# Optimization experiments

Measured on AMD Instinct MI355X. Metric: run time of the kernel, lower is better.

## Reference

```python
import jax, jax.numpy as jnp
import numpy as np

B, S, H = 4, 2048, 1024
E, K, INTER = 16, 2, 512
ALPHA, LIMIT = 1.702, 7.0


def setup_inputs() -> dict:
    key = jax.random.key(0)
    ks = jax.random.split(key, 6)
    return {
        "hidden_states": jax.random.normal(ks[0], (B, S, H), jnp.float32),
        "router_weight": jax.random.normal(ks[1], (H, E), jnp.float32) * 0.02,
        "gate_up_proj": jax.random.normal(ks[2], (E, H, 2 * INTER), jnp.float32) * 0.02,
        "gate_up_proj_bias": jax.random.normal(ks[3], (E, 2 * INTER), jnp.float32) * 0.02,
        "down_proj": jax.random.normal(ks[4], (E, INTER, H), jnp.float32) * 0.02,
        "down_proj_bias": jax.random.normal(ks[5], (E, H), jnp.float32) * 0.02,
    }


def reference(hidden_states, router_weight, gate_up_proj, gate_up_proj_bias,
              down_proj, down_proj_bias):
    b, s, h = hidden_states.shape
    x = hidden_states.reshape(-1, h)  # [T, H]
    # Router: linear logits -> top-k -> softmax over selected -> sparse scores [T, E]
    logits = x @ router_weight                      # [T, E]
    topk_w, topk_i = jax.lax.top_k(logits, K)       # [T, K]
    topk_w = jax.nn.softmax(topk_w, axis=-1)
    one_hot = (topk_i[..., None] == jnp.arange(E)[None, None, :]).astype(topk_w.dtype)
    scores = jnp.einsum('tk,tke->te', topk_w, one_hot)  # [T, E]
    # Fused gate+up projection per expert (num_devices=1 => dispatch/combine identity)
    gu = jnp.einsum('th,ehf->tef', x, gate_up_proj) + gate_up_proj_bias  # [T, E, 2I]
    gate = gu[..., ::2]   # interleaved layout
    up = gu[..., 1::2]
    # gpt_oss activation: clamp + scaled sigmoid glu
    gate = jnp.minimum(gate, LIMIT)
    up = jnp.clip(up, -LIMIT, LIMIT)
    glu = gate * jax.nn.sigmoid(gate * ALPHA)
    act = (up + 1.0) * glu                          # [T, E, I]
    # Down projection + score-weighted combine
    out = jnp.einsum('tei,eih,te->th', act, down_proj, scores)
    out = out + jnp.einsum('te,eh->th', scores, down_proj_bias)
    return out.reshape(b, s, h)
```

## Files before the change

kernel.cpp:

```cpp
#include <hip/hip_runtime.h>
#include <hip/hip_bf16.h>
#include <math.h>

#define TOK   8192
#define HDIM  1024
#define NE    16
#define NI    512
#define F2    1024
#define CAP   8192
#define CAP2  2048
#define ALPHA 1.702f
#define LIMIT 7.0f

typedef __attribute__((ext_vector_type(8))) short short8;
typedef __attribute__((ext_vector_type(4))) short short4v;
typedef __attribute__((ext_vector_type(4))) float f32x4;

static __device__ __forceinline__ unsigned short f2bf(float f) {
    unsigned int u = __float_as_uint(f);
    u += 0x7FFFu + ((u >> 16) & 1u);
    return (unsigned short)(u >> 16);
}
static __device__ __forceinline__ float bf2f(unsigned short u) {
    return __uint_as_float((unsigned int)u << 16);
}

#define GLD_LDS16(g, l) __builtin_amdgcn_global_load_lds(                     \
    (const __attribute__((address_space(1))) void*)(g),                       \
    (__attribute__((address_space(3))) void*)(l), 16, 0, 0)

static __device__ __forceinline__ void do_transpose256(
    const float* __restrict__ in, unsigned short* __restrict__ out,
    int R, int C, int perm, int e, int bx, int by, char* smem, int tid)
{
    unsigned short (*t2)[264] = (unsigned short (*)[264])smem;
    const float* pin = in + (size_t)e * R * C;
    unsigned short* pout = out + (size_t)e * R * C;
    int c0 = bx * 64, r0 = by * 256;

#pragma unroll
    for (int j = 0; j < 8; ++j) {
        int idx = j * 256 + tid;
        int rp = idx >> 4, c4 = (idx & 15) * 4;
        int swz = ((c4 >> 2) & 7) << 3;
        const float* p0 = pin + (size_t)(r0 + 2 * rp) * C + c0 + c4;
        float4 v0 = *(const float4*)(p0);
        float4 v1 = *(const float4*)(p0 + C);
        unsigned int u0 = (unsigned int)f2bf(v0.x) | ((unsigned int)f2bf(v1.x) << 16);
        unsigned int u1 = (unsigned int)f2bf(v0.y) | ((unsigned int)f2bf(v1.y) << 16);
        unsigned int u2 = (unsigned int)f2bf(v0.z) | ((unsigned int)f2bf(v1.z) << 16);
        unsigned int u3 = (unsigned int)f2bf(v0.w) | ((unsigned int)f2bf(v1.w) << 16);
        int kc = (2 * rp) ^ swz;
        *(unsigned int*)&t2[c4 + 0][kc] = u0;
        *(unsigned int*)&t2[c4 + 1][kc] = u1;
        *(unsigned int*)&t2[c4 + 2][kc] = u2;
        *(unsigned int*)&t2[c4 + 3][kc] = u3;
    }
    __syncthreads();

#pragma unroll
    for (int j = 0; j < 8; ++j) {
        int idx = j * 256 + tid;
        int n = idx >> 5, k0 = (idx & 31) * 8;
        int rswz = ((n >> 2) & 7) << 3;
        short8 v = *(const short8*)&t2[n][k0 ^ rswz];
        int c = c0 + n;
        int orow;
        if (perm) {
            int tile = c >> 7, ct = c & 127;
            int fl = ct >> 1, h = ct & 1;
            orow = (tile << 7) | ((fl >> 4) << 5) | (h << 4) | (fl & 15);
        } else {
            orow = c;
        }
        *(short8*)(pout + (size_t)orow * R + r0 + k0) = v;
    }
}

__global__ __launch_bounds__(256) void prep_kernel(
    const float* __restrict__ x, const float* __restrict__ rw,
    const float* __restrict__ gup,
    double* __restrict__ part, unsigned short* __restrict__ xbf,
    unsigned short* __restrict__ gupT)
{
    __shared__ __align__(16) char smem[33792];
    int bid = blockIdx.x;
    int tid = threadIdx.x;

    if (bid >= 512) {
        int i = bid - 512;
        do_transpose256(gup, gupT, HDIM, F2, 1, i >> 6, i & 15, (i >> 4) & 3, smem, tid);
        return;
    }

    int idx = bid;
    int w = tid >> 6;
    int lane = tid & 63;
    int tt = lane & 15, eg = lane >> 4;
    int t0 = idx * 16;
    int hbase = w * 256;

    float* sx  = (float*)(smem + w * 8448);
    float* srw = (float*)(smem + w * 8448 + 4352);

    double acc[4] = {0.0, 0.0, 0.0, 0.0};

    for (int hc = 0; hc < 4; ++hc) {
        int h0 = hbase + hc * 64;
        __syncthreads();
#pragma unroll
        for (int j = 0; j < 4; ++j) {
            int fidx = j * 64 + lane;
            int t = fidx >> 4, c4 = (fidx & 15) * 4;
            float4 v = *(const float4*)(x + (size_t)(t0 + t) * HDIM + h0 + c4);
            *(float4*)&sx[t * 68 + c4] = v;
            short4v s;
            s[0] = (short)f2bf(v.x); s[1] = (short)f2bf(v.y);
            s[2] = (short)f2bf(v.z); s[3] = (short)f2bf(v.w);
            *(short4v*)(xbf + (size_t)(t0 + t) * HDIM + h0 + c4) = s;
        }
#pragma unroll
        for (int j = 0; j < 4; ++j) {
            int ridx = j * 64 + lane;
            int h = ridx >> 2, e4 = (ridx & 3) * 4;
            float4 v = *(const float4*)(rw + (size_t)(h0 + h) * NE + e4);
            *(float4*)&srw[h * 16 + e4] = v;
        }
        __syncthreads();
#pragma unroll 8
        for (int j = 0; j < 64; ++j) {
            float xv = sx[tt * 68 + j];
            float4 wv = *(const float4*)&srw[j * 16 + eg * 4];
            double xd = (double)xv;
            acc[0] += xd * (double)wv.x;
            acc[1] += xd * (double)wv.y;
            acc[2] += xd * (double)wv.z;
            acc[3] += xd * (double)wv.w;
        }
    }
#pragma unroll
    for (int q = 0; q < 4; ++q)
        part[(size_t)(w * NE + eg * 4 + q) * TOK + t0 + tt] = acc[q];
}

__global__ __launch_bounds__(256) void router_combine_kernel(
    const double* __restrict__ part,
    int* __restrict__ counts, int* __restrict__ toks, float* __restrict__ wgts,
    unsigned short* __restrict__ inv)
{
    __shared__ int lhist[NE];
    __shared__ int lbase[NE];
    int tid = threadIdx.x;
    int t = blockIdx.x * 256 + tid;
    if (tid < NE) lhist[tid] = 0;
    __syncthreads();

    double acc[NE];
#pragma unroll
    for (int e = 0; e < NE; ++e)
        acc[e] = part[(size_t)(0 * NE + e) * TOK + t]
               + part[(size_t)(1 * NE + e) * TOK + t]
               + part[(size_t)(2 * NE + e) * TOK + t]
               + part[(size_t)(3 * NE + e) * TOK + t];

    int i0 = 0; double v0 = acc[0];
#pragma unroll
    for (int e = 1; e < NE; ++e) if (acc[e] > v0) { v0 = acc[e]; i0 = e; }
    int i1 = -1; double v1 = -1e300;
#pragma unroll
    for (int e = 0; e < NE; ++e) if (e != i0 && acc[e] > v1) { v1 = acc[e]; i1 = e; }
    double e1 = exp(v1 - v0);
    float w0 = (float)(1.0 / (1.0 + e1));
    float w1 = (float)(e1 / (1.0 + e1));

    int r0 = atomicAdd(&lhist[i0], 1);
    int r1 = atomicAdd(&lhist[i1], 1);
    __syncthreads();
    if (tid < NE) lbase[tid] = atomicAdd(&counts[tid], lhist[tid]);
    __syncthreads();
    int p0 = lbase[i0] + r0; if (p0 > 2047) p0 = 2047;
    int p1 = lbase[i1] + r1; if (p1 > 2047) p1 = 2047;
    toks[i0 * CAP + p0] = t; wgts[i0 * CAP + p0] = w0;
    toks[i1 * CAP + p1] = t; wgts[i1 * CAP + p1] = w1;
    inv[2 * t]     = (unsigned short)((i0 << 11) | p0);
    inv[2 * t + 1] = (unsigned short)((i1 << 11) | p1);
}

#define KLOOP_BODY(NT, KOFF)                                                          \
    int c0 = 0;                                                                       \
    for (int kb = 0; kb < (NT); ++kb) {                                               \
        if (kb + 2 < (NT)) {                                                          \
            int cpre = c0 + 2; if (cpre >= 3) cpre -= 3;                              \
            _Pragma("unroll")                                                         \
            for (int i = 0; i < 2; ++i) {                                             \
                GLD_LDS16(gaA[i] + (kb + 2) * (KOFF), &As[cpre][w * 32 + i * 16][0]); \
                GLD_LDS16(gaB[i] + (kb + 2) * (KOFF), &Bs[cpre][w * 32 + i * 16][0]); \
            }                                                                         \
            asm volatile("s_waitcnt vmcnt(8)" ::: "memory");                          \
        } else if (kb + 1 < (NT)) {                                                   \
            asm volatile("s_waitcnt vmcnt(4)" ::: "memory");                          \
        } else {                                                                      \
            asm volatile("s_waitcnt vmcnt(0)" ::: "memory");                          \
        }                                                                             \
        __builtin_amdgcn_sched_barrier(0);                                            \
        __builtin_amdgcn_s_barrier();                                                 \
        __builtin_amdgcn_sched_barrier(0);                                            \
        short8 af[4], bfr[4];                                                         \
        _Pragma("unroll")                                                             \
        for (int m = 0; m < 4; ++m) af[m] = *(const short8*)&As[c0][wr * 64 + m * 16 + lr][slt]; \
        _Pragma("unroll")                                                             \
        for (int n = 0; n < 4; ++n) bfr[n] = *(const short8*)&Bs[c0][wc * 64 + n * 16 + lr][slt]; \
        _Pragma("unroll")                                                             \
        for (int m = 0; m < 4; ++m)                                                   \
            _Pragma("unroll")                                                         \
            for (int n = 0; n < 4; ++n)                                               \
                acc[m][n] = __builtin_amdgcn_mfma_f32_16x16x32_bf16(af[m], bfr[n], acc[m][n], 0, 0, 0); \
        asm volatile("s_waitcnt lgkmcnt(0)" ::: "memory");                            \
        __builtin_amdgcn_sched_barrier(0);                                            \
        __builtin_amdgcn_s_barrier();                                                 \
        __builtin_amdgcn_sched_barrier(0);                                            \
        c0 = (c0 + 1 == 3) ? 0 : c0 + 1;                                              \
    }

#define KLOOP_PROLOGUE(KOFF)                                                          \
    _Pragma("unroll")                                                                 \
    for (int i = 0; i < 2; ++i) {                                                     \
        GLD_LDS16(gaA[i], &As[0][w * 32 + i * 16][0]);                                \
        GLD_LDS16(gaB[i], &Bs[0][w * 32 + i * 16][0]);                                \
    }                                                                                 \
    _Pragma("unroll")                                                                 \
    for (int i = 0; i < 2; ++i) {                                                     \
        GLD_LDS16(gaA[i] + (KOFF), &As[1][w * 32 + i * 16][0]);                       \
        GLD_LDS16(gaB[i] + (KOFF), &Bs[1][w * 32 + i * 16][0]);                       \
    }

__global__ __launch_bounds__(256) void gemm1_kernel(
    const unsigned short* __restrict__ xb, const unsigned short* __restrict__ gupT,
    const float* __restrict__ gub,
    const int* __restrict__ counts, const int* __restrict__ toks,
    unsigned short* __restrict__ act, const unsigned short* __restrict__ zp,
    const float* __restrict__ dwn, unsigned short* __restrict__ dwnT)
{
    __shared__ __align__(16) char smem[49664];
    int b = blockIdx.x;
    int tid = threadIdx.x;

    if (b >= 2048) {
        int i = b - 2048;
        do_transpose256(dwn, dwnT, NI, HDIM, 0, i >> 5, i & 15, (i >> 4) & 1, smem, tid);
        return;
    }

    unsigned short (*As)[128][32] = (unsigned short (*)[128][32])smem;
    unsigned short (*Bs)[128][32] = (unsigned short (*)[128][32])(smem + 24576);
    int* rtok = (int*)(smem + 49152);

    int e = b & 15;
    int j = b >> 4;
    int nt = j & 7;
    int mt = j >> 3;
    int cnt = counts[e];
    int row0 = mt * 128;
    if (row0 >= cnt) return;
    int n0 = nt * 128;

    int lane = tid & 63;
    int w = tid >> 6;
    int wr = w >> 1, wc = w & 1;
    int lr = lane & 15, lg = lane >> 4;

    if (tid < 128) {
        int p = row0 + tid;
        rtok[tid] = (p < cnt) ? toks[e * CAP + p] : -1;
    }
    __syncthreads();

    int srow = lane >> 2;
    int scol = (((lane & 3) ^ ((lane >> 3) & 3)) * 8);
    int slt = (lg ^ ((lr >> 1) & 3)) * 8;

    const unsigned short* gaA[2];
    const unsigned short* gaB[2];
    const unsigned short* gupE = gupT + (size_t)e * HDIM * F2;
#pragma unroll
    for (int i = 0; i < 2; ++i) {
        int arow = w * 32 + i * 16 + srow;
        int tk = rtok[arow];
        gaA[i] = (tk >= 0) ? (xb + (size_t)tk * HDIM + scol) : (zp + scol);
        int brow = n0 + w * 32 + i * 16 + srow;
        gaB[i] = gupE + (size_t)brow * HDIM + scol;
    }

    f32x4 acc[4][4];
#pragma unroll
    for (int m = 0; m < 4; ++m)
#pragma unroll
        for (int n = 0; n < 4; ++n) acc[m][n] = (f32x4){0.f, 0.f, 0.f, 0.f};

    KLOOP_PROLOGUE(32)
    KLOOP_BODY(HDIM / 32, 32)

    unsigned short* actE = act + (size_t)e * CAP2 * NI;
    int fbase = nt * 64 + wc * 32;
#pragma unroll
    for (int q = 0; q < 2; ++q) {
        int f = fbase + q * 16 + lr;
        float bg = gub[e * F2 + 2 * f];
        float bu = gub[e * F2 + 2 * f + 1];
#pragma unroll
        for (int m = 0; m < 4; ++m) {
#pragma unroll
            for (int r = 0; r < 4; ++r) {
                float gate = acc[m][2 * q][r] + bg;
                float up   = acc[m][2 * q + 1][r] + bu;
                gate = fminf(gate, LIMIT);
                up   = fminf(fmaxf(up, -LIMIT), LIMIT);
                float glu = gate / (1.0f + __expf(-ALPHA * gate));
                float av  = (up + 1.0f) * glu;
                int row = row0 + wr * 64 + m * 16 + lg * 4 + r;
                actE[(size_t)row * NI + f] = f2bf(av);
            }
        }
    }
}

__global__ __launch_bounds__(256) void gemm2_y_kernel(
    const unsigned short* __restrict__ act, const unsigned short* __restrict__ dwnT,
    const float* __restrict__ dwb,
    const int* __restrict__ counts, const float* __restrict__ wgts,
    unsigned short* __restrict__ y)
{
    int b = blockIdx.x;
    int e = b & 15;
    int j = b >> 4;
    int nt = j & 7;
    int mt = j >> 3;
    int cnt = counts[e];
    int row0 = mt * 128;
    if (row0 >= cnt) return;
    int n0 = nt * 128;

    int base_e = 0;
#pragma unroll
    for (int q = 0; q < NE; ++q) base_e += (q < e) ? counts[q] : 0;

    __shared__ __align__(16) unsigned short As[3][128][32];
    __shared__ __align__(16) unsigned short Bs[3][128][32];
    __shared__ float rwgt[128];

    int tid = threadIdx.x;
    int lane = tid & 63;
    int w = tid >> 6;
    int wr = w >> 1, wc = w & 1;
    int lr = lane & 15, lg = lane >> 4;

    if (tid < 128) {
        int p = row0 + tid;
        rwgt[tid] = (p < cnt) ? wgts[e * CAP + p] : 0.0f;
    }
    __syncthreads();

    int srow = lane >> 2;
    int scol = (((lane & 3) ^ ((lane >> 3) & 3)) * 8);
    int slt = (lg ^ ((lr >> 1) & 3)) * 8;

    const unsigned short* gaA[2];
    const unsigned short* gaB[2];
    const unsigned short* actE = act + (size_t)e * CAP2 * NI;
    const unsigned short* dwnE = dwnT + (size_t)e * HDIM * NI;
#pragma unroll
    for (int i = 0; i < 2; ++i) {
        int arow = row0 + w * 32 + i * 16 + srow;
        gaA[i] = actE + (size_t)arow * NI + scol;
        int brow = n0 + w * 32 + i * 16 + srow;
        gaB[i] = dwnE + (size_t)brow * NI + scol;
    }

    f32x4 acc[4][4];
#pragma unroll
    for (int m = 0; m < 4; ++m)
#pragma unroll
        for (int n = 0; n < 4; ++n) acc[m][n] = (f32x4){0.f, 0.f, 0.f, 0.f};

    KLOOP_PROLOGUE(32)
    KLOOP_BODY(NI / 32, 32)

    unsigned short* yB = y + (size_t)(base_e + row0) * HDIM;
#pragma unroll
    for (int n = 0; n < 4; ++n) {
        int hc = n0 + wc * 64 + n * 16 + lr;
        float db = dwb[e * HDIM + hc];
#pragma unroll
        for (int m = 0; m < 4; ++m) {
#pragma unroll
            for (int r = 0; r < 4; ++r) {
                int rl = wr * 64 + m * 16 + lg * 4 + r;
                if (row0 + rl < cnt)
                    yB[(size_t)rl * HDIM + hc] = f2bf(rwgt[rl] * (acc[m][n][r] + db));
            }
        }
    }
}

__global__ __launch_bounds__(256) void out_combine_kernel(
    const unsigned short* __restrict__ y, const unsigned short* __restrict__ inv,
    const int* __restrict__ counts, float* __restrict__ out)
{
    __shared__ int sbase[NE];
    int tid = threadIdx.x;
    int t = blockIdx.x;
    if (tid == 0) {
        int s = 0;
#pragma unroll
        for (int e = 0; e < NE; ++e) { sbase[e] = s; s += counts[e]; }
    }
    __syncthreads();
    unsigned short v0 = inv[2 * t], v1 = inv[2 * t + 1];
    int s0 = sbase[v0 >> 11] + (v0 & 2047);
    int s1 = sbase[v1 >> 11] + (v1 & 2047);
    short4v a = *(const short4v*)(y + (size_t)s0 * HDIM + tid * 4);
    short4v c = *(const short4v*)(y + (size_t)s1 * HDIM + tid * 4);
    float4 o;
    o.x = bf2f((unsigned short)a[0]) + bf2f((unsigned short)c[0]);
    o.y = bf2f((unsigned short)a[1]) + bf2f((unsigned short)c[1]);
    o.z = bf2f((unsigned short)a[2]) + bf2f((unsigned short)c[2]);
    o.w = bf2f((unsigned short)a[3]) + bf2f((unsigned short)c[3]);
    *(float4*)(out + (size_t)t * HDIM + tid * 4) = o;
}

__global__ __launch_bounds__(256) void router_kernel(
    const float* __restrict__ x, const float* __restrict__ rw,
    int* __restrict__ counts, int* __restrict__ toks, float* __restrict__ wgts)
{
    int gwave = (int)((blockIdx.x * 256 + threadIdx.x) >> 6);
    int lane = threadIdx.x & 63;
    if (gwave >= TOK) return;
    const float* xr = x + (size_t)gwave * HDIM;
    double acc[NE];
#pragma unroll
    for (int e = 0; e < NE; ++e) acc[e] = 0.0;
    for (int i = 0; i < HDIM / 64; ++i) {
        int h = i * 64 + lane;
        double xv = (double)xr[h];
        const float* r = rw + (size_t)h * NE;
#pragma unroll
        for (int e = 0; e < NE; ++e) acc[e] += xv * (double)r[e];
    }
#pragma unroll
    for (int e = 0; e < NE; ++e) {
        double v = acc[e];
#pragma unroll
        for (int off = 32; off > 0; off >>= 1) v += __shfl_xor(v, off);
        acc[e] = v;
    }
    if (lane == 0) {
        int i0 = 0; double v0 = acc[0];
#pragma unroll
        for (int e = 1; e < NE; ++e) if (acc[e] > v0) { v0 = acc[e]; i0 = e; }
        int i1 = -1; double v1 = -1e300;
#pragma unroll
        for (int e = 0; e < NE; ++e) if (e != i0 && acc[e] > v1) { v1 = acc[e]; i1 = e; }
        double e1 = exp(v1 - v0);
        float w0 = (float)(1.0 / (1.0 + e1));
        float w1 = (float)(e1 / (1.0 + e1));
        int p0 = atomicAdd(&counts[i0], 1);
        toks[i0 * CAP + p0] = gwave; wgts[i0 * CAP + p0] = w0;
        int p1 = atomicAdd(&counts[i1], 1);
        toks[i1 * CAP + p1] = gwave; wgts[i1 * CAP + p1] = w1;
    }
}

__global__ __launch_bounds__(256) void moe_kernel(
    const float* __restrict__ x,
    const float* __restrict__ gup, const float* __restrict__ gub,
    const float* __restrict__ dwn, const float* __restrict__ dwb,
    const int* __restrict__ counts, const int* __restrict__ toks,
    const float* __restrict__ wgts, float* __restrict__ out)
{
    int e = blockIdx.y;
    int cnt = counts[e];
    int row0 = blockIdx.x * 64;
    if (row0 >= cnt) return;

    __shared__ __align__(16) unsigned short sA[64][40];
    __shared__ __align__(16) unsigned short sB[64][40];
    __shared__ __align__(16) unsigned short sAct[64][520];
    __shared__ int   rtok[64];
    __shared__ float rwgt[64];

    int tid = threadIdx.x;
    if (tid < 64) {
        int idx = row0 + tid;
        bool v = idx < cnt;
        rtok[tid] = v ? toks[e * CAP + idx] : -1;
        rwgt[tid] = v ? wgts[e * CAP + idx] : 0.0f;
    }
    __syncthreads();

    int lane = tid & 63;
    int w = tid >> 6;
    int wr = w >> 1, wc = w & 1;
    int lr = lane & 15, lg = lane >> 4;
    int ar = tid >> 2, ac0 = (tid & 3) * 8;
    int bk = tid >> 3, bf0 = (tid & 7) * 8;
    const float* gupE = gup + (size_t)e * HDIM * F2;

    for (int nb = 0; nb < F2 / 64; ++nb) {
        f32x4 acc[2][2];
#pragma unroll
        for (int mi = 0; mi < 2; ++mi)
#pragma unroll
            for (int ni = 0; ni < 2; ++ni) acc[mi][ni] = (f32x4){0.f, 0.f, 0.f, 0.f};
        for (int kb = 0; kb < HDIM / 32; ++kb) {
            __syncthreads();
            {
                int tk = rtok[ar];
                short8 vv = {0,0,0,0,0,0,0,0};
                if (tk >= 0) {
                    const float* p = x + (size_t)tk * HDIM + kb * 32 + ac0;
                    float4 u0 = *(const float4*)(p); float4 u1 = *(const float4*)(p + 4);
                    vv[0]=(short)f2bf(u0.x); vv[1]=(short)f2bf(u0.y); vv[2]=(short)f2bf(u0.z); vv[3]=(short)f2bf(u0.w);
                    vv[4]=(short)f2bf(u1.x); vv[5]=(short)f2bf(u1.y); vv[6]=(short)f2bf(u1.z); vv[7]=(short)f2bf(u1.w);
                }
                *(short8*)&sA[ar][ac0] = vv;
            }
            {
                const float* p = gupE + (size_t)(kb * 32 + bk) * F2 + nb * 64 + bf0;
                float4 u0 = *(const float4*)(p); float4 u1 = *(const float4*)(p + 4);
                sB[bf0+0][bk]=f2bf(u0.x); sB[bf0+1][bk]=f2bf(u0.y); sB[bf0+2][bk]=f2bf(u0.z); sB[bf0+3][bk]=f2bf(u0.w);
                sB[bf0+4][bk]=f2bf(u1.x); sB[bf0+5][bk]=f2bf(u1.y); sB[bf0+6][bk]=f2bf(u1.z); sB[bf0+7][bk]=f2bf(u1.w);
            }
            __syncthreads();
            short8 a0 = *(const short8*)&sA[wr*32+lr][lg*8];
            short8 a1 = *(const short8*)&sA[wr*32+16+lr][lg*8];
            short8 b0 = *(const short8*)&sB[wc*32+lr][lg*8];
            short8 b1 = *(const short8*)&sB[wc*32+16+lr][lg*8];
            acc[0][0] = __builtin_amdgcn_mfma_f32_16x16x32_bf16(a0,b0,acc[0][0],0,0,0);
            acc[0][1] = __builtin_amdgcn_mfma_f32_16x16x32_bf16(a0,b1,acc[0][1],0,0,0);
            acc[1][0] = __builtin_amdgcn_mfma_f32_16x16x32_bf16(a1,b0,acc[1][0],0,0,0);
            acc[1][1] = __builtin_amdgcn_mfma_f32_16x16x32_bf16(a1,b1,acc[1][1],0,0,0);
        }
#pragma unroll
        for (int ni = 0; ni < 2; ++ni) {
            int fc = nb * 64 + wc * 32 + ni * 16 + lr;
            float bias = gub[e * F2 + fc];
#pragma unroll
            for (int mi = 0; mi < 2; ++mi)
#pragma unroll
                for (int r = 0; r < 4; ++r) {
                    float gu = acc[mi][ni][r] + bias;
                    float other = __shfl_xor(gu, 1);
                    float gate = (lr & 1) ? other : gu;
                    float up   = (lr & 1) ? gu : other;
                    gate = fminf(gate, LIMIT);
                    up = fminf(fmaxf(up, -LIMIT), LIMIT);
                    float glu = gate / (1.0f + __expf(-ALPHA * gate));
                    float av = (up + 1.0f) * glu;
                    if (!(lr & 1)) sAct[wr*32+mi*16+lg*4+r][fc >> 1] = f2bf(av);
                }
        }
    }
    __syncthreads();

    const float* dwnE = dwn + (size_t)e * NI * HDIM;
    int tks[2][4]; float wvs[2][4];
#pragma unroll
    for (int mi = 0; mi < 2; ++mi)
#pragma unroll
        for (int r = 0; r < 4; ++r) {
            int row = wr*32 + mi*16 + lg*4 + r;
            tks[mi][r] = rtok[row]; wvs[mi][r] = rwgt[row];
        }
    for (int nb = 0; nb < HDIM / 64; ++nb) {
        f32x4 acc[2][2];
#pragma unroll
        for (int mi = 0; mi < 2; ++mi)
#pragma unroll
            for (int ni = 0; ni < 2; ++ni) acc[mi][ni] = (f32x4){0.f,0.f,0.f,0.f};
        for (int kb = 0; kb < NI / 32; ++kb) {
            __syncthreads();
            {
                const float* p = dwnE + (size_t)(kb*32 + bk) * HDIM + nb*64 + bf0;
                float4 u0 = *(const float4*)(p); float4 u1 = *(const float4*)(p + 4);
                sB[bf0+0][bk]=f2bf(u0.x); sB[bf0+1][bk]=f2bf(u0.y); sB[bf0+2][bk]=f2bf(u0.z); sB[bf0+3][bk]=f2bf(u0.w);
                sB[bf0+4][bk]=f2bf(u1.x); sB[bf0+5][bk]=f2bf(u1.y); sB[bf0+6][bk]=f2bf(u1.z); sB[bf0+7][bk]=f2bf(u1.w);
            }
            __syncthreads();
            short8 a0 = *(const short8*)&sAct[wr*32+lr][kb*32+lg*8];
            short8 a1 = *(const short8*)&sAct[wr*32+16+lr][kb*32+lg*8];
            short8 b0 = *(const short8*)&sB[wc*32+lr][lg*8];
            short8 b1 = *(const short8*)&sB[wc*32+16+lr][lg*8];
            acc[0][0] = __builtin_amdgcn_mfma_f32_16x16x32_bf16(a0,b0,acc[0][0],0,0,0);
            acc[0][1] = __builtin_amdgcn_mfma_f32_16x16x32_bf16(a0,b1,acc[0][1],0,0,0);
            acc[1][0] = __builtin_amdgcn_mfma_f32_16x16x32_bf16(a1,b0,acc[1][0],0,0,0);
            acc[1][1] = __builtin_amdgcn_mfma_f32_16x16x32_bf16(a1,b1,acc[1][1],0,0,0);
        }
#pragma unroll
        for (int ni = 0; ni < 2; ++ni) {
            int hc = nb*64 + wc*32 + ni*16 + lr;
            float db = dwb[e * HDIM + hc];
#pragma unroll
            for (int mi = 0; mi < 2; ++mi)
#pragma unroll
                for (int r = 0; r < 4; ++r) {
                    int tk = tks[mi][r];
                    if (tk >= 0)
                        atomicAdd(out + (size_t)tk * HDIM + hc, wvs[mi][r] * (acc[mi][ni][r] + db));
                }
        }
    }
}

extern "C" void kernel_launch(void* const* d_in, const int* in_sizes, int n_in,
                              void* d_out, int out_size, void* d_ws, size_t ws_size,
                              hipStream_t stream) {
    const float* x   = (const float*)d_in[0];
    const float* rw  = (const float*)d_in[1];
    const float* gup = (const float*)d_in[2];
    const float* gub = (const float*)d_in[3];
    const float* dwn = (const float*)d_in[4];
    const float* dwb = (const float*)d_in[5];
    float* out = (float*)d_out;

    const size_t OFF_COUNTS = 0;
    const size_t OFF_ZP     = 256;
    const size_t OFF_INV    = 4352;
    const size_t OFF_TOKS   = OFF_INV  + (size_t)TOK * 2 * 2;
    const size_t OFF_WGTS   = OFF_TOKS + (size_t)NE * CAP * 4;
    const size_t OFF_DWNT   = OFF_WGTS + (size_t)NE * CAP * 4;
    const size_t OFF_ACT    = OFF_DWNT + (size_t)NE * NI * HDIM * 2;
    const size_t OFF_XBF    = OFF_ACT  + (size_t)NE * CAP2 * NI * 2;
    const size_t OFF_GUPT   = OFF_XBF  + (size_t)TOK * HDIM * 2;
    const size_t REQ_B      = OFF_GUPT + (size_t)NE * HDIM * F2 * 2;
    const size_t OFF_Y      = OFF_XBF;
    const size_t REQ_A      = OFF_Y + (size_t)2 * TOK * HDIM * 2;

    if (ws_size >= REQ_B) {
        int*            counts = (int*)((char*)d_ws + OFF_COUNTS);
        unsigned short* zp     = (unsigned short*)((char*)d_ws + OFF_ZP);
        unsigned short* inv    = (unsigned short*)((char*)d_ws + OFF_INV);
        int*            toks   = (int*)((char*)d_ws + OFF_TOKS);
        float*          wgts   = (float*)((char*)d_ws + OFF_WGTS);
        unsigned short* dwnT   = (unsigned short*)((char*)d_ws + OFF_DWNT);
        unsigned short* act    = (unsigned short*)((char*)d_ws + OFF_ACT);
        double*         part   = (double*)((char*)d_ws + OFF_ACT);
        unsigned short* xbf    = (unsigned short*)((char*)d_ws + OFF_XBF);
        unsigned short* gupT   = (unsigned short*)((char*)d_ws + OFF_GUPT);
        unsigned short* y      = (unsigned short*)((char*)d_ws + OFF_Y);

        hipMemsetAsync(d_ws, 0, 4352, stream);

        prep_kernel<<<512 + 1024, 256, 0, stream>>>(x, rw, gup, part, xbf, gupT);

        router_combine_kernel<<<TOK / 256, 256, 0, stream>>>(part, counts, toks, wgts, inv);

        gemm1_kernel<<<2048 + 512, 256, 0, stream>>>(xbf, gupT, gub, counts, toks, act, zp,
                                                     dwn, dwnT);
        int g2 = (CAP2 / 128) * (HDIM / 128) * NE;

        if (ws_size >= REQ_A) {
            gemm2_y_kernel<<<g2, 256, 0, stream>>>(act, dwnT, dwb, counts, wgts, y);
            out_combine_kernel<<<TOK, 256, 0, stream>>>(y, inv, counts, out);
        } else {
            hipMemsetAsync(d_out, 0, (size_t)out_size * sizeof(float), stream);
            out_combine_kernel<<<TOK, 256, 0, stream>>>(y, inv, counts, out);
        }
    } else {
        int*   counts = (int*)d_ws;
        int*   toks   = (int*)((char*)d_ws + 64);
        float* wgts   = (float*)((char*)d_ws + 64 + (size_t)NE * CAP * sizeof(int));
        hipMemsetAsync(d_ws, 0, 64, stream);
        hipMemsetAsync(d_out, 0, (size_t)out_size * sizeof(float), stream);
        router_kernel<<<TOK / 4, 256, 0, stream>>>(x, rw, counts, toks, wgts);
        dim3 gm(TOK / 64, NE);
        moe_kernel<<<gm, 256, 0, stream>>>(x, gup, gub, dwn, dwb, counts, toks, wgts, out);
    }
}
```

Baseline: 151.0 us.

## Switch expert GEMMs to BK=64 double-buffered pipeline with wider swizzle

Both expert GEMM kernels move from a triple-buffered BK=32 K-loop with a two-stage prefetch to a double-buffered BK=64 loop. Each stage now loads four 16-byte rows per thread and the LDS swizzle is widened to eight 16-byte chunks. The aim is to halve the number of barrier pairs per tile and raise the MFMA work done between syncs. In exchange, prefetch depth drops to one stage and LDS use grows to about 64 KB per block, which may reduce occupancy.

```diff
diff --git a/kernel.cpp b/kernel.cpp
--- a/kernel.cpp
+++ b/kernel.cpp
@@ -186,52 +186,45 @@
     inv[2 * t + 1] = (unsigned short)((i1 << 11) | p1);
 }
 
-#define KLOOP_BODY(NT, KOFF)                                                          \
-    int c0 = 0;                                                                       \
+#define STAGE64(buf, kidx)                                                            \
+    _Pragma("unroll")                                                                 \
+    for (int q = 0; q < 4; ++q) {                                                     \
+        GLD_LDS16(gaA[q] + (size_t)(kidx) * 64, &As[buf][q * 32 + w * 8][0]);         \
+        GLD_LDS16(gaB[q] + (size_t)(kidx) * 64, &Bs[buf][q * 32 + w * 8][0]);         \
+    }
+
+#define KLOOP64_BODY(NT)                                                              \
+    int cb = 0;                                                                       \
     for (int kb = 0; kb < (NT); ++kb) {                                               \
-        if (kb + 2 < (NT)) {                                                          \
-            int cpre = c0 + 2; if (cpre >= 3) cpre -= 3;                              \
-            _Pragma("unroll")                                                         \
-            for (int i = 0; i < 2; ++i) {                                             \
-                GLD_LDS16(gaA[i] + (kb + 2) * (KOFF), &As[cpre][w * 32 + i * 16][0]); \
-                GLD_LDS16(gaB[i] + (kb + 2) * (KOFF), &Bs[cpre][w * 32 + i * 16][0]); \
-            }                                                                         \
+        if (kb + 1 < (NT)) {                                                          \
+            STAGE64(cb ^ 1, kb + 1)                                                   \
             asm volatile("s_waitcnt vmcnt(8)" ::: "memory");                          \
-        } else if (kb + 1 < (NT)) {                                                   \
-            asm volatile("s_waitcnt vmcnt(4)" ::: "memory");                          \
         } else {                                                                      \
             asm volatile("s_waitcnt vmcnt(0)" ::: "memory");                          \
         }                                                                             \
         __builtin_amdgcn_sched_barrier(0);                                            \
         __builtin_amdgcn_s_barrier();                                                 \
         __builtin_amdgcn_sched_barrier(0);                                            \
-        short8 af[4], bfr[4];                                                         \
         _Pragma("unroll")                                                             \
-        for (int m = 0; m < 4; ++m) af[m] = *(const short8*)&As[c0][wr * 64 + m * 16 + lr][slt]; \
-        _Pragma("unroll")                                                             \
-        for (int n = 0; n < 4; ++n) bfr[n] = *(const short8*)&Bs[c0][wc * 64 + n * 16 + lr][slt]; \
-        _Pragma("unroll")                                                             \
-        for (int m = 0; m < 4; ++m)                                                   \
+        for (int ks = 0; ks < 2; ++ks) {                                              \
+            short8 af[4], bfr[4];                                                     \
+            _Pragma("unroll")                                                         \
+            for (int m = 0; m < 4; ++m)                                               \
+                af[m] = *(const short8*)&As[cb][wr * 64 + m * 16 + lr][kch[ks]];      \
             _Pragma("unroll")                                                         \
             for (int n = 0; n < 4; ++n)                                               \
-                acc[m][n] = __builtin_amdgcn_mfma_f32_16x16x32_bf16(af[m], bfr[n], acc[m][n], 0, 0, 0); \
+                bfr[n] = *(const short8*)&Bs[cb][wc * 64 + n * 16 + lr][kch[ks]];     \
+            _Pragma("unroll")                                                         \
+            for (int m = 0; m < 4; ++m)                                               \
+                _Pragma("unroll")                                                     \
+                for (int n = 0; n < 4; ++n)                                           \
+                    acc[m][n] = __builtin_amdgcn_mfma_f32_16x16x32_bf16(af[m], bfr[n], acc[m][n], 0, 0, 0); \
+        }                                                                             \
         asm volatile("s_waitcnt lgkmcnt(0)" ::: "memory");                            \
         __builtin_amdgcn_sched_barrier(0);                                            \
         __builtin_amdgcn_s_barrier();                                                 \
         __builtin_amdgcn_sched_barrier(0);                                            \
-        c0 = (c0 + 1 == 3) ? 0 : c0 + 1;                                              \
-    }
-
-#define KLOOP_PROLOGUE(KOFF)                                                          \
-    _Pragma("unroll")                                                                 \
-    for (int i = 0; i < 2; ++i) {                                                     \
-        GLD_LDS16(gaA[i], &As[0][w * 32 + i * 16][0]);                                \
-        GLD_LDS16(gaB[i], &Bs[0][w * 32 + i * 16][0]);                                \
-    }                                                                                 \
-    _Pragma("unroll")                                                                 \
-    for (int i = 0; i < 2; ++i) {                                                     \
-        GLD_LDS16(gaA[i] + (KOFF), &As[1][w * 32 + i * 16][0]);                       \
-        GLD_LDS16(gaB[i] + (KOFF), &Bs[1][w * 32 + i * 16][0]);                       \
+        cb ^= 1;                                                                      \
     }
 
 __global__ __launch_bounds__(256) void gemm1_kernel(
@@ -241,7 +234,7 @@
     unsigned short* __restrict__ act, const unsigned short* __restrict__ zp,
     const float* __restrict__ dwn, unsigned short* __restrict__ dwnT)
 {
-    __shared__ __align__(16) char smem[49664];
+    __shared__ __align__(16) char smem[66048];
     int b = blockIdx.x;
     int tid = threadIdx.x;
 
@@ -251,9 +244,9 @@
         return;
     }
 
-    unsigned short (*As)[128][32] = (unsigned short (*)[128][32])smem;
-    unsigned short (*Bs)[128][32] = (unsigned short (*)[128][32])(smem + 24576);
-    int* rtok = (int*)(smem + 49152);
+    unsigned short (*As)[128][64] = (unsigned short (*)[128][64])smem;
+    unsigned short (*Bs)[128][64] = (unsigned short (*)[128][64])(smem + 32768);
+    int* rtok = (int*)(smem + 65536);
 
     int e = b & 15;
     int j = b >> 4;
@@ -275,20 +268,20 @@
     }
     __syncthreads();
 
-    int srow = lane >> 2;
-    int scol = (((lane & 3) ^ ((lane >> 3) & 3)) * 8);
-    int slt = (lg ^ ((lr >> 1) & 3)) * 8;
-
-    const unsigned short* gaA[2];
-    const unsigned short* gaB[2];
+    int srow8 = lane >> 3;
+    int scq   = ((lane & 7) ^ srow8) * 8;
+    int kch[2] = { ((0 + lg) ^ (lr & 7)) * 8, ((4 + lg) ^ (lr & 7)) * 8 };
+
+    const unsigned short* gaA[4];
+    const unsigned short* gaB[4];
     const unsigned short* gupE = gupT + (size_t)e * HDIM * F2;
 #pragma unroll
-    for (int i = 0; i < 2; ++i) {
-        int arow = w * 32 + i * 16 + srow;
-        int tk = rtok[arow];
-        gaA[i] = (tk >= 0) ? (xb + (size_t)tk * HDIM + scol) : (zp + scol);
-        int brow = n0 + w * 32 + i * 16 + srow;
-        gaB[i] = gupE + (size_t)brow * HDIM + scol;
+    for (int q = 0; q < 4; ++q) {
+        int ar = q * 32 + w * 8 + srow8;
+        int tk = rtok[ar];
+        gaA[q] = (tk >= 0) ? (xb + (size_t)tk * HDIM + scq) : (zp + scq);
+        int br = n0 + q * 32 + w * 8 + srow8;
+        gaB[q] = gupE + (size_t)br * HDIM + scq;
     }
 
     f32x4 acc[4][4];
@@ -297,8 +290,8 @@
 #pragma unroll
         for (int n = 0; n < 4; ++n) acc[m][n] = (f32x4){0.f, 0.f, 0.f, 0.f};
 
-    KLOOP_PROLOGUE(32)
-    KLOOP_BODY(HDIM / 32, 32)
+    STAGE64(0, 0)
+    KLOOP64_BODY(HDIM / 64)
 
     unsigned short* actE = act + (size_t)e * CAP2 * NI;
     int fbase = nt * 64 + wc * 32;
@@ -344,8 +337,8 @@
 #pragma unroll
     for (int q = 0; q < NE; ++q) base_e += (q < e) ? counts[q] : 0;
 
-    __shared__ __align__(16) unsigned short As[3][128][32];
-    __shared__ __align__(16) unsigned short Bs[3][128][32];
+    __shared__ __align__(16) unsigned short As[2][128][64];
+    __shared__ __align__(16) unsigned short Bs[2][128][64];
     __shared__ float rwgt[128];
 
     int tid = threadIdx.x;
@@ -360,20 +353,20 @@
     }
     __syncthreads();
 
-    int srow = lane >> 2;
-    int scol = (((lane & 3) ^ ((lane >> 3) & 3)) * 8);
-    int slt = (lg ^ ((lr >> 1) & 3)) * 8;
-
-    const unsigned short* gaA[2];
-    const unsigned short* gaB[2];
+    int srow8 = lane >> 3;
+    int scq   = ((lane & 7) ^ srow8) * 8;
+    int kch[2] = { ((0 + lg) ^ (lr & 7)) * 8, ((4 + lg) ^ (lr & 7)) * 8 };
+
+    const unsigned short* gaA[4];
+    const unsigned short* gaB[4];
     const unsigned short* actE = act + (size_t)e * CAP2 * NI;
     const unsigned short* dwnE = dwnT + (size_t)e * HDIM * NI;
 #pragma unroll
-    for (int i = 0; i < 2; ++i) {
-        int arow = row0 + w * 32 + i * 16 + srow;
-        gaA[i] = actE + (size_t)arow * NI + scol;
-        int brow = n0 + w * 32 + i * 16 + srow;
-        gaB[i] = dwnE + (size_t)brow * NI + scol;
+    for (int q = 0; q < 4; ++q) {
+        int ar = row0 + q * 32 + w * 8 + srow8;
+        gaA[q] = actE + (size_t)ar * NI + scq;
+        int br = n0 + q * 32 + w * 8 + srow8;
+        gaB[q] = dwnE + (size_t)br * NI + scq;
     }
 
     f32x4 acc[4][4];
@@ -382,8 +375,8 @@
 #pragma unroll
         for (int n = 0; n < 4; ++n) acc[m][n] = (f32x4){0.f, 0.f, 0.f, 0.f};
 
-    KLOOP_PROLOGUE(32)
-    KLOOP_BODY(NI / 32, 32)
+    STAGE64(0, 0)
+    KLOOP64_BODY(NI / 64)
 
     unsigned short* yB = y + (size_t)(base_e + row0) * HDIM;
 #pragma unroll
```

After: 159.1 us. 1.05x slower.
